# Kernel tuning notes

Measured on AMD Instinct MI355X. Metric: run time of the kernel, lower is better.

Reference implementation:

```python
import jax, jax.numpy as jnp
import numpy as np

B, N, NPOINT, K = 16, 4096, 1024, 8
CIN, COUT = 128, 256
RADIUS = 0.2
BN_EPS = 1e-5


def fps(pts, npoint):
    # pts: [B, N, 3] -> indices [B, npoint], farthest point sampling starting at index 0
    b, n, _ = pts.shape

    def body(carry, _):
        dists, last = carry  # dists [B,N], last [B]
        cur = jnp.take_along_axis(pts, last[:, None, None], axis=1)  # [B,1,3]
        d = jnp.sum((pts - cur) ** 2, axis=-1)  # [B,N]
        dists = jnp.minimum(dists, d)
        nxt = jnp.argmax(dists, axis=-1).astype(jnp.int32)
        return (dists, nxt), last

    init = (jnp.full((b, n), jnp.finfo(pts.dtype).max, pts.dtype),
            jnp.zeros((b,), jnp.int32))
    _, idxs = jax.lax.scan(body, init, None, length=npoint)  # [npoint, B]
    return idxs.T  # [B, npoint]


def ball_query(new_xyz, pts, radius, k):
    # new_xyz [B,S,3], pts [B,N,3] -> idx [B,S,k] (pad with first in-ball index, pointnet2 semantics)
    n = pts.shape[1]
    d2 = jnp.sum((new_xyz[:, :, None, :] - pts[:, None, :, :]) ** 2, axis=-1)  # [B,S,N]
    cand = jnp.where(d2 <= radius * radius, jnp.arange(n, dtype=jnp.int32), n)
    idx = jnp.sort(cand, axis=-1)[..., :k]  # first k in-ball indices (center always in-ball)
    idx = jnp.where(idx == n, idx[..., :1], idx)
    return idx


def setup_inputs() -> dict:
    key = jax.random.key(0)
    ks = jax.random.split(key, 8)
    xyz = jax.random.uniform(ks[0], (B, 3, N), dtype=jnp.float32)
    feat = jax.random.normal(ks[1], (B, CIN, N), dtype=jnp.float32)
    conv_w = jax.random.normal(ks[2], (COUT, CIN), dtype=jnp.float32) * (1.0 / np.sqrt(CIN))
    conv_b = jax.random.normal(ks[3], (COUT,), dtype=jnp.float32) * 0.01
    bn_gamma = jax.random.uniform(ks[4], (COUT,), dtype=jnp.float32, minval=0.5, maxval=1.5)
    bn_beta = jax.random.normal(ks[5], (COUT,), dtype=jnp.float32) * 0.1
    bn_mean = jax.random.normal(ks[6], (COUT,), dtype=jnp.float32) * 0.1
    bn_var = jax.random.uniform(ks[7], (COUT,), dtype=jnp.float32, minval=0.5, maxval=1.5)
    return {"xyz": xyz, "feat": feat, "conv_w": conv_w, "conv_b": conv_b,
            "bn_gamma": bn_gamma, "bn_beta": bn_beta, "bn_mean": bn_mean, "bn_var": bn_var}


def reference(xyz, feat, conv_w, conv_b, bn_gamma, bn_beta, bn_mean, bn_var):
    pts = jnp.transpose(xyz, (0, 2, 1))   # [B,N,3]
    fts = jnp.transpose(feat, (0, 2, 1))  # [B,N,F]

    fps_idx = fps(pts, NPOINT)                                        # [B,S]
    new_xyz = jnp.take_along_axis(pts, fps_idx[..., None], axis=1)    # [B,S,3]

    idx = ball_query(new_xyz, pts, RADIUS, K)                          # [B,S,K]
    grouped = jax.vmap(lambda f, i: f[i])(fts, idx)                    # [B,S,K,F]

    # shared pointwise Conv1d (kernel 1) + BatchNorm (inference stats) + ReLU
    x = jnp.einsum('bskf,of->bsko', grouped, conv_w) + conv_b          # [B,S,K,COUT]
    x = bn_gamma * (x - bn_mean) / jnp.sqrt(bn_var + BN_EPS) + bn_beta
    x = jax.nn.relu(x)
    new_feat = jnp.max(x, axis=2)                                      # [B,S,COUT]
    return new_xyz, new_feat
```

## Files before the change

kernel.cpp:

```cpp
#include <hip/hip_runtime.h>
#include <hip/hip_bf16.h>
#include <stdint.h>

#define Bn   16
#define Nn   4096
#define Sn   1024
#define Kn   8
#define CINn 128
#define COUTn 256

static __device__ __forceinline__ float sqdist(float ax, float ay, float az,
                                               float bx, float by, float bz) {
    float dx = __fsub_rn(ax, bx);
    float dy = __fsub_rn(ay, by);
    float dz = __fsub_rn(az, bz);
    return __fadd_rn(__fadd_rn(__fmul_rn(dx, dx), __fmul_rn(dy, dy)), __fmul_rn(dz, dz));
}

static __device__ __forceinline__ unsigned long long u64max(unsigned long long a,
                                                            unsigned long long b) {
    return a > b ? a : b;
}

#define DPP_MAX_LEVEL(lo, hi, CTRL)                                              \
    do {                                                                         \
        int _olo = __builtin_amdgcn_update_dpp(lo, lo, CTRL, 0xF, 0xF, false);   \
        int _ohi = __builtin_amdgcn_update_dpp(hi, hi, CTRL, 0xF, 0xF, false);   \
        unsigned long long _o = ((unsigned long long)(unsigned)_ohi << 32) |     \
                                (unsigned)_olo;                                  \
        unsigned long long _k = ((unsigned long long)(unsigned)hi << 32) |       \
                                (unsigned)lo;                                    \
        if (_o > _k) { lo = _olo; hi = _ohi; }                                   \
    } while (0)

static __device__ __forceinline__ unsigned long long wave_max_u64(unsigned long long key) {
    int lo = (int)(unsigned)(key & 0xFFFFFFFFull);
    int hi = (int)(unsigned)(key >> 32);
    DPP_MAX_LEVEL(lo, hi, 0x111);
    DPP_MAX_LEVEL(lo, hi, 0x112);
    DPP_MAX_LEVEL(lo, hi, 0x114);
    DPP_MAX_LEVEL(lo, hi, 0x118);
    DPP_MAX_LEVEL(lo, hi, 0x142);
    DPP_MAX_LEVEL(lo, hi, 0x143);
    unsigned flo = (unsigned)__builtin_amdgcn_readlane(lo, 63);
    unsigned fhi = (unsigned)__builtin_amdgcn_readlane(hi, 63);
    return ((unsigned long long)fhi << 32) | flo;
}

__global__ __launch_bounds__(256) void k_fps(const float* __restrict__ xyz,
                                             float* __restrict__ out_xyz) {
    __shared__ __align__(16) float xs[Nn], ys[Nn], zs[Nn];
    __shared__ __align__(16) unsigned long long gbuf[2][4];
    const int b = blockIdx.x;
    const int tid = threadIdx.x;
    const int wid = tid >> 6, lane = tid & 63;
    const float* base = xyz + (size_t)b * 3 * Nn;
    for (int i = tid; i < Nn; i += 256) {
        xs[i] = base[i];
        ys[i] = base[Nn + i];
        zs[i] = base[2 * Nn + i];
    }
    __syncthreads();
    float px[16], py[16], pz[16], dist[16];
#pragma unroll
    for (int j = 0; j < 16; ++j) {
        int p = tid + j * 256;
        px[j] = xs[p]; py[j] = ys[p]; pz[j] = zs[p];
        dist[j] = 3.402823466e+38f;
    }
    int last = 0;
    if (tid == 0) {
        out_xyz[(size_t)(b * Sn) * 3 + 0] = xs[0];
        out_xyz[(size_t)(b * Sn) * 3 + 1] = ys[0];
        out_xyz[(size_t)(b * Sn) * 3 + 2] = zs[0];
    }
    for (int s = 1; s < Sn; ++s) {
        const float cx = xs[last], cy = ys[last], cz = zs[last];
        float mv = -1.0f; int mi = 0;
#pragma unroll
        for (int j = 0; j < 16; ++j) {
            float d = sqdist(px[j], py[j], pz[j], cx, cy, cz);
            float nd = fminf(dist[j], d);
            dist[j] = nd;
            if (nd > mv) { mv = nd; mi = tid + j * 256; }
        }
        unsigned long long key =
            ((unsigned long long)__float_as_uint(mv) << 32) | (unsigned)(Nn - 1 - mi);
        key = wave_max_u64(key);
        if (lane == 0) gbuf[s & 1][wid] = key;
        __syncthreads();
        const ulonglong2 g0 = *(const ulonglong2*)&gbuf[s & 1][0];
        const ulonglong2 g1 = *(const ulonglong2*)&gbuf[s & 1][2];
        key = u64max(u64max(g0.x, g0.y), u64max(g1.x, g1.y));
        const int nl = Nn - 1 - (int)(unsigned)(key & 0xFFFFFFFFull);
        if (tid == 0) {
            out_xyz[(size_t)(b * Sn + s) * 3 + 0] = xs[nl];
            out_xyz[(size_t)(b * Sn + s) * 3 + 1] = ys[nl];
            out_xyz[(size_t)(b * Sn + s) * 3 + 2] = zs[nl];
        }
        last = nl;
    }
}

static __device__ __forceinline__ void wave_ball(const float* __restrict__ base,
                                                 float cx, float cy, float cz,
                                                 int lane, int* bslot) {
    int cnt = 0;
    int idx0 = -1;
    for (int chunk = 0; chunk < Nn / 64; ++chunk) {
        const int p = chunk * 64 + lane;
        const float d2 = sqdist(base[p], base[Nn + p], base[2 * Nn + p], cx, cy, cz);
        const bool in = (d2 <= 0.04f);
        const unsigned long long m = __ballot(in);
        if (m != 0ull) {
            if (idx0 < 0) idx0 = chunk * 64 + __builtin_ctzll(m);
            const int rank = cnt + __popcll(m & ((1ull << lane) - 1ull));
            if (in && rank < Kn)
                bslot[rank] = p;
            cnt += __popcll(m);
            if (cnt >= Kn) break;
        }
    }
    if (lane < Kn && lane >= cnt)
        bslot[lane] = idx0;
}

__global__ __launch_bounds__(1024) void k_feat(const float* __restrict__ xyz,
                                               const float* __restrict__ out_xyz,
                                               const float* __restrict__ feat,
                                               const float* __restrict__ conv_w,
                                               const float* __restrict__ conv_b,
                                               const float* __restrict__ bn_g,
                                               const float* __restrict__ bn_b,
                                               const float* __restrict__ bn_m,
                                               const float* __restrict__ bn_v,
                                               float* __restrict__ out_feat) {
    __shared__ float Wlds[CINn][COUTn + 1];
    __shared__ int bidx[16][Kn];
    const int tid = threadIdx.x;
    const int wave = tid >> 6, lane = tid & 63;
    const int b  = blockIdx.x & 15;
    const int c0 = (blockIdx.x >> 4) * 16;
    const int bs = b * Sn + c0 + wave;

    {
        const float4* cw4 = (const float4*)conv_w;
#pragma unroll
        for (int i = 0; i < 8; ++i) {
            const int idx = tid + 1024 * i;
            const float4 v = cw4[idx];
            const int o = idx >> 5, f4 = idx & 31;
            Wlds[f4 * 4 + 0][o] = v.x;
            Wlds[f4 * 4 + 1][o] = v.y;
            Wlds[f4 * 4 + 2][o] = v.z;
            Wlds[f4 * 4 + 3][o] = v.w;
        }
    }

    const float* base = xyz + (size_t)b * 3 * Nn;
    const float cx = out_xyz[(size_t)bs * 3 + 0];
    const float cy = out_xyz[(size_t)bs * 3 + 1];
    const float cz = out_xyz[(size_t)bs * 3 + 2];
    wave_ball(base, cx, cy, cz, lane, &bidx[wave][0]);

    int pt[Kn];
#pragma unroll
    for (int k = 0; k < Kn; ++k) pt[k] = bidx[wave][k];

    __syncthreads();

    const float* fb = feat + (size_t)b * CINn * Nn;
    float acc[4][Kn];
#pragma unroll
    for (int j = 0; j < 4; ++j)
#pragma unroll
        for (int k = 0; k < Kn; ++k) acc[j][k] = 0.0f;

    for (int f4 = 0; f4 < CINn / 4; ++f4) {
#pragma unroll
        for (int c = 0; c < 4; ++c) {
            const float* frc = fb + (size_t)(f4 * 4 + c) * Nn;
            float fv[Kn];
#pragma unroll
            for (int k = 0; k < Kn; ++k) fv[k] = frc[pt[k]];
#pragma unroll
            for (int j = 0; j < 4; ++j) {
                const float wc = Wlds[f4 * 4 + c][lane + 64 * j];
#pragma unroll
                for (int k = 0; k < Kn; ++k) acc[j][k] += fv[k] * wc;
            }
        }
    }

#pragma unroll
    for (int j = 0; j < 4; ++j) {
        const int o = lane + 64 * j;
        const float bias = conv_b[o];
        const float g = bn_g[o], be = bn_b[o], mn = bn_m[o], vr = bn_v[o];
        const float inv = sqrtf(vr + 1e-5f);
        float mx = -3.402823466e+38f;
#pragma unroll
        for (int k = 0; k < Kn; ++k) {
            float z = acc[j][k] + bias;
            float y = g * (z - mn) / inv + be;
            y = fmaxf(y, 0.0f);
            mx = fmaxf(mx, y);
        }
        out_feat[(size_t)bs * COUTn + o] = mx;
    }
}

extern "C" void kernel_launch(void* const* d_in, const int* in_sizes, int n_in,
                              void* d_out, int out_size, void* d_ws, size_t ws_size,
                              hipStream_t stream) {
    const float* xyz    = (const float*)d_in[0];
    const float* feat   = (const float*)d_in[1];
    const float* conv_w = (const float*)d_in[2];
    const float* conv_b = (const float*)d_in[3];
    const float* bn_g   = (const float*)d_in[4];
    const float* bn_b   = (const float*)d_in[5];
    const float* bn_m   = (const float*)d_in[6];
    const float* bn_v   = (const float*)d_in[7];

    float* out_xyz  = (float*)d_out;
    float* out_feat = out_xyz + (size_t)Bn * Sn * 3;

    k_fps <<<dim3(Bn),            dim3(256),  0, stream>>>(xyz, out_xyz);
    k_feat<<<dim3(Bn * Sn / 16),  dim3(1024), 0, stream>>>(xyz, out_xyz, feat,
                                                           conv_w, conv_b,
                                                           bn_g, bn_b, bn_m, bn_v,
                                                           out_feat);
}
```

Baseline: 829.2 us.

## Widen FPS to 512 threads and stage gathered features in LDS for conv

FPS now runs with 512 threads and 8 points per thread, cutting the serial per-iteration loop length at the cost of a wider cross-wave reduction. The feature kernel shrinks to 512-thread blocks handling 8 centers. It gathers each wave's neighbor features cooperatively (32 channels x 8 neighbors per chunk) into an LDS tile with register prefetch of the next chunk. It then reads them as float4 alongside register-cached weight rows, replacing per-lane scalar global gathers. The aim is fewer redundant scattered global loads and more FMA reuse per LDS read, with added LDS usage and pressure on registers.

After: 905.1 us. 9.2% more time.

```diff
diff --git a/kernel.cpp b/kernel.cpp
--- a/kernel.cpp
+++ b/kernel.cpp
@@ -47,24 +47,24 @@
     return ((unsigned long long)fhi << 32) | flo;
 }
 
-__global__ __launch_bounds__(256) void k_fps(const float* __restrict__ xyz,
+__global__ __launch_bounds__(512) void k_fps(const float* __restrict__ xyz,
                                              float* __restrict__ out_xyz) {
     __shared__ __align__(16) float xs[Nn], ys[Nn], zs[Nn];
-    __shared__ __align__(16) unsigned long long gbuf[2][4];
+    __shared__ __align__(16) unsigned long long gbuf[2][8];
     const int b = blockIdx.x;
     const int tid = threadIdx.x;
     const int wid = tid >> 6, lane = tid & 63;
     const float* base = xyz + (size_t)b * 3 * Nn;
-    for (int i = tid; i < Nn; i += 256) {
+    for (int i = tid; i < Nn; i += 512) {
         xs[i] = base[i];
         ys[i] = base[Nn + i];
         zs[i] = base[2 * Nn + i];
     }
     __syncthreads();
-    float px[16], py[16], pz[16], dist[16];
-#pragma unroll
-    for (int j = 0; j < 16; ++j) {
-        int p = tid + j * 256;
+    float px[8], py[8], pz[8], dist[8];
+#pragma unroll
+    for (int j = 0; j < 8; ++j) {
+        int p = tid + j * 512;
         px[j] = xs[p]; py[j] = ys[p]; pz[j] = zs[p];
         dist[j] = 3.402823466e+38f;
     }
@@ -78,20 +78,21 @@
         const float cx = xs[last], cy = ys[last], cz = zs[last];
         float mv = -1.0f; int mi = 0;
 #pragma unroll
-        for (int j = 0; j < 16; ++j) {
+        for (int j = 0; j < 8; ++j) {
             float d = sqdist(px[j], py[j], pz[j], cx, cy, cz);
             float nd = fminf(dist[j], d);
             dist[j] = nd;
-            if (nd > mv) { mv = nd; mi = tid + j * 256; }
+            if (nd > mv) { mv = nd; mi = tid + j * 512; }
         }
         unsigned long long key =
             ((unsigned long long)__float_as_uint(mv) << 32) | (unsigned)(Nn - 1 - mi);
         key = wave_max_u64(key);
         if (lane == 0) gbuf[s & 1][wid] = key;
         __syncthreads();
-        const ulonglong2 g0 = *(const ulonglong2*)&gbuf[s & 1][0];
-        const ulonglong2 g1 = *(const ulonglong2*)&gbuf[s & 1][2];
-        key = u64max(u64max(g0.x, g0.y), u64max(g1.x, g1.y));
+        const ulonglong2* gb = (const ulonglong2*)&gbuf[s & 1][0];
+        const ulonglong2 g0 = gb[0], g1 = gb[1], g2 = gb[2], g3 = gb[3];
+        key = u64max(u64max(u64max(g0.x, g0.y), u64max(g1.x, g1.y)),
+                     u64max(u64max(g2.x, g2.y), u64max(g3.x, g3.y)));
         const int nl = Nn - 1 - (int)(unsigned)(key & 0xFFFFFFFFull);
         if (tid == 0) {
             out_xyz[(size_t)(b * Sn + s) * 3 + 0] = xs[nl];
@@ -125,29 +126,30 @@
         bslot[lane] = idx0;
 }
 
-__global__ __launch_bounds__(1024) void k_feat(const float* __restrict__ xyz,
-                                               const float* __restrict__ out_xyz,
-                                               const float* __restrict__ feat,
-                                               const float* __restrict__ conv_w,
-                                               const float* __restrict__ conv_b,
-                                               const float* __restrict__ bn_g,
-                                               const float* __restrict__ bn_b,
-                                               const float* __restrict__ bn_m,
-                                               const float* __restrict__ bn_v,
-                                               float* __restrict__ out_feat) {
+__global__ __launch_bounds__(512) void k_feat(const float* __restrict__ xyz,
+                                              const float* __restrict__ out_xyz,
+                                              const float* __restrict__ feat,
+                                              const float* __restrict__ conv_w,
+                                              const float* __restrict__ conv_b,
+                                              const float* __restrict__ bn_g,
+                                              const float* __restrict__ bn_b,
+                                              const float* __restrict__ bn_m,
+                                              const float* __restrict__ bn_v,
+                                              float* __restrict__ out_feat) {
     __shared__ float Wlds[CINn][COUTn + 1];
-    __shared__ int bidx[16][Kn];
+    __shared__ __align__(16) float At[8][Kn][36];
+    __shared__ int bidx[8][Kn];
     const int tid = threadIdx.x;
     const int wave = tid >> 6, lane = tid & 63;
     const int b  = blockIdx.x & 15;
-    const int c0 = (blockIdx.x >> 4) * 16;
+    const int c0 = (blockIdx.x >> 4) * 8;
     const int bs = b * Sn + c0 + wave;
 
     {
         const float4* cw4 = (const float4*)conv_w;
 #pragma unroll
-        for (int i = 0; i < 8; ++i) {
-            const int idx = tid + 1024 * i;
+        for (int i = 0; i < 16; ++i) {
+            const int idx = tid + 512 * i;
             const float4 v = cw4[idx];
             const int o = idx >> 5, f4 = idx & 31;
             Wlds[f4 * 4 + 0][o] = v.x;
@@ -170,24 +172,60 @@
     __syncthreads();
 
     const float* fb = feat + (size_t)b * CINn * Nn;
+    const int fl = lane & 31;
+    const int kh = lane >> 5;
+
     float acc[4][Kn];
 #pragma unroll
     for (int j = 0; j < 4; ++j)
 #pragma unroll
         for (int k = 0; k < Kn; ++k) acc[j][k] = 0.0f;
 
-    for (int f4 = 0; f4 < CINn / 4; ++f4) {
-#pragma unroll
-        for (int c = 0; c < 4; ++c) {
-            const float* frc = fb + (size_t)(f4 * 4 + c) * Nn;
-            float fv[Kn];
-#pragma unroll
-            for (int k = 0; k < Kn; ++k) fv[k] = frc[pt[k]];
-#pragma unroll
-            for (int j = 0; j < 4; ++j) {
-                const float wc = Wlds[f4 * 4 + c][lane + 64 * j];
-#pragma unroll
-                for (int k = 0; k < Kn; ++k) acc[j][k] += fv[k] * wc;
+    float stg[4];
+#pragma unroll
+    for (int kk = 0; kk < 4; ++kk) {
+        const int ptk = kh ? pt[kk * 2 + 1] : pt[kk * 2];
+        stg[kk] = fb[(size_t)fl * Nn + ptk];
+    }
+
+#pragma unroll
+    for (int fc = 0; fc < 4; ++fc) {
+#pragma unroll
+        for (int kk = 0; kk < 4; ++kk)
+            At[wave][kk * 2 + kh][fl] = stg[kk];
+        if (fc < 3) {
+#pragma unroll
+            for (int kk = 0; kk < 4; ++kk) {
+                const int ptk = kh ? pt[kk * 2 + 1] : pt[kk * 2];
+                stg[kk] = fb[(size_t)((fc + 1) * 32 + fl) * Nn + ptk];
+            }
+        }
+#pragma unroll
+        for (int f4l = 0; f4l < 8; ++f4l) {
+            const int f4 = fc * 8 + f4l;
+            float wreg[4][4];
+#pragma unroll
+            for (int c = 0; c < 4; ++c) {
+                const float* wrow = &Wlds[f4 * 4 + c][lane];
+                wreg[c][0] = wrow[0];
+                wreg[c][1] = wrow[64];
+                wreg[c][2] = wrow[128];
+                wreg[c][3] = wrow[192];
+            }
+#pragma unroll
+            for (int khf = 0; khf < 2; ++khf) {
+                float4 fv4[4];
+#pragma unroll
+                for (int kk = 0; kk < 4; ++kk)
+                    fv4[kk] = *(const float4*)&At[wave][khf * 4 + kk][f4l * 4];
+#pragma unroll
+                for (int c = 0; c < 4; ++c)
+#pragma unroll
+                    for (int j = 0; j < 4; ++j)
+#pragma unroll
+                        for (int kk = 0; kk < 4; ++kk)
+                            acc[j][khf * 4 + kk] +=
+                                ((const float*)&fv4[kk])[c] * wreg[c][j];
             }
         }
     }
@@ -225,9 +263,9 @@
     float* out_xyz  = (float*)d_out;
     float* out_feat = out_xyz + (size_t)Bn * Sn * 3;
 
-    k_fps <<<dim3(Bn),            dim3(256),  0, stream>>>(xyz, out_xyz);
-    k_feat<<<dim3(Bn * Sn / 16),  dim3(1024), 0, stream>>>(xyz, out_xyz, feat,
-                                                           conv_w, conv_b,
-                                                           bn_g, bn_b, bn_m, bn_v,
-                                                           out_feat);
-}
+    k_fps <<<dim3(Bn),           dim3(512), 0, stream>>>(xyz, out_xyz);
+    k_feat<<<dim3(Bn * Sn / 8),  dim3(512), 0, stream>>>(xyz, out_xyz, feat,
+                                                         conv_w, conv_b,
+                                                         bn_g, bn_b, bn_m, bn_v,
+                                                         out_feat);
+}
```
